# Optimization experiments

Hardware: AMD Instinct MI355X
Metric: run time of the kernel (lower is better)

Reference implementation:

```python
import jax, jax.numpy as jnp
import numpy as np

EMBED_DIM = 768
NUM_HEADS = 12
HEAD_DIM = EMBED_DIM // NUM_HEADS
SCALER = HEAD_DIM ** (-0.5)


def setup_inputs() -> dict:
    key = jax.random.key(0)
    k_x, k_wqkv, k_wo = jax.random.split(key, 3)
    B, N, C = 8, 1024, EMBED_DIM
    # GlorotUniform limits
    lim_qkv = (6.0 / (C + 3 * C)) ** 0.5
    lim_o = (6.0 / (C + C)) ** 0.5
    return {
        "inputs": jax.random.normal(k_x, (B, N, C), dtype=jnp.float32),
        "w_qkv": jax.random.uniform(k_wqkv, (C, 3 * C), minval=-lim_qkv, maxval=lim_qkv, dtype=jnp.float32),
        "b_qkv": jnp.zeros((3 * C,), dtype=jnp.float32),
        "w_out": jax.random.uniform(k_wo, (C, C), minval=-lim_o, maxval=lim_o, dtype=jnp.float32),
        "b_out": jnp.zeros((C,), dtype=jnp.float32),
    }


def reference(inputs, w_qkv, b_qkv, w_out, b_out):
    B, N, C = inputs.shape
    H, D = NUM_HEADS, C // NUM_HEADS
    qkv = inputs @ w_qkv + b_qkv                      # [B, N, 3C]
    qkv = qkv.reshape(B, N, 3, H, D).transpose(2, 0, 3, 1, 4)  # [3, B, H, N, D]
    q, k, v = qkv[0], qkv[1], qkv[2]
    scores = jnp.einsum("bhnd,bhmd->bhnm", q, k) * SCALER      # [B, H, N, N]
    attn = jax.nn.softmax(scores, axis=-1)
    x = jnp.einsum("bhnm,bhmd->bhnd", attn, v)                  # [B, H, N, D]
    x = x.transpose(0, 2, 1, 3).reshape(B, N, C)
    return x @ w_out + b_out
```

## Files before the change

### kernel.cpp

```cpp
#include <hip/hip_runtime.h>
#include <hip/hip_bf16.h>
#include <cstdint>
#include <cstddef>

#define EMBED 768
#define NHEADS 12
#define HDIM 64
#define SEQ 1024
#define BATCH 8

typedef __attribute__((ext_vector_type(8))) short bf16x8;
typedef __attribute__((ext_vector_type(4))) float f32x4;
typedef __attribute__((ext_vector_type(16))) float f32x16;
typedef __attribute__((ext_vector_type(4))) unsigned int u32x4;

__device__ __forceinline__ short f2bf(float f) {
    union { float f; uint32_t u; } x; x.f = f;
    uint32_t r = x.u + 0x7fffu + ((x.u >> 16) & 1u);
    return (short)(r >> 16);
}

__device__ __forceinline__ unsigned int cvt_pk_bf16(float lo, float hi) {
    unsigned int r;
    asm("v_cvt_pk_bf16_f32 %0, %1, %2" : "=v"(r) : "v"(lo), "v"(hi));
    return r;
}

__device__ __forceinline__ void permswap(unsigned int& a, unsigned int& b) {
    asm volatile("v_permlane32_swap_b32 %0, %1" : "+v"(a), "+v"(b));
}

__device__ __forceinline__ void gload_lds16(const void* g, void* l) {
    __builtin_amdgcn_global_load_lds(
        (const __attribute__((address_space(1))) unsigned int*)g,
        (__attribute__((address_space(3))) unsigned int*)l, 16, 0, 0);
}

__global__ __launch_bounds__(256) void prep(
    const float* __restrict__ x, short* __restrict__ Xbf,
    const float* __restrict__ w_qkv, short* __restrict__ wqkvT,
    const float* __restrict__ w_out, short* __restrict__ woutT) {
    __shared__ float tile[64][65];
    const int tid = threadIdx.x;
    const int bidx = blockIdx.x;
    if (bidx < 3072) {
        size_t i = ((size_t)bidx * 256 + tid) * 8;
        float4 a = *reinterpret_cast<const float4*>(x + i);
        float4 b = *reinterpret_cast<const float4*>(x + i + 4);
        bf16x8 v;
        v[0] = f2bf(a.x); v[1] = f2bf(a.y); v[2] = f2bf(a.z); v[3] = f2bf(a.w);
        v[4] = f2bf(b.x); v[5] = f2bf(b.y); v[6] = f2bf(b.z); v[7] = f2bf(b.w);
        *reinterpret_cast<bf16x8*>(Xbf + i) = v;
        return;
    }
    const float* in;
    short* out;
    int R, C, c0, r0;
    if (bidx < 3504) {
        int bid = bidx - 3072;
        in = w_qkv; out = wqkvT; R = 768; C = 2304;
        c0 = (bid % 36) * 64; r0 = (bid / 36) * 64;
    } else {
        int bid = bidx - 3504;
        in = w_out; out = woutT; R = 768; C = 768;
        c0 = (bid % 12) * 64; r0 = (bid / 12) * 64;
    }
#pragma unroll
    for (int i = 0; i < 16; ++i) {
        int e = tid + 256 * i;
        int r = e >> 6, c = e & 63;
        tile[r][c] = in[(size_t)(r0 + r) * C + c0 + c];
    }
    __syncthreads();
#pragma unroll
    for (int i = 0; i < 16; ++i) {
        int e = tid + 256 * i;
        int rr = e >> 6, cc = e & 63;
        out[(size_t)(c0 + rr) * R + r0 + cc] = f2bf(tile[cc][rr]);
    }
}

__global__ __launch_bounds__(512) void gemm_qkv(
    const short* __restrict__ A, const short* __restrict__ Bt,
    const float* __restrict__ bias,
    short* __restrict__ Qo, short* __restrict__ Ko, short* __restrict__ Vto) {
    __shared__ __align__(16) char smem[65536];
    const int tid = threadIdx.x;
    const int lane = tid & 63;
    const int wid = tid >> 6;
    const int wm = wid >> 1, wn = wid & 1;
    const int bid = blockIdx.x;
    const int wg = (bid & 7) * 144 + (bid >> 3);
    const int mb = wg / 18, nb = wg - mb * 18;
    const int m0 = mb * 128;
    const int n0 = nb * 128;

    const f32x4 zero4 = {0.f, 0.f, 0.f, 0.f};
    f32x4 acc[2][4];
#pragma unroll
    for (int i = 0; i < 2; ++i)
#pragma unroll
        for (int j = 0; j < 4; ++j) acc[i][j] = zero4;

    const short* Ab = A + (size_t)m0 * EMBED;
    const short* Bb = Bt + (size_t)n0 * EMBED;

    auto stage = [&](int p, int kt) {
        const int k0 = kt * 64;
        char* base = smem + p * 32768;
#pragma unroll
        for (int i = 0; i < 2; ++i) {
            int e = i * 512 + tid;
            int r = e >> 3, cs = (e & 7) ^ (r & 7);
            char* dst = base + (size_t)(i * 512 + wid * 64) * 16;
            gload_lds16(Ab + (size_t)r * EMBED + k0 + cs * 8, dst);
            gload_lds16(Bb + (size_t)r * EMBED + k0 + cs * 8, dst + 16384);
        }
    };

    stage(0, 0);
    stage(1, 1);
    asm volatile("s_waitcnt vmcnt(4)" ::: "memory");
    __builtin_amdgcn_s_barrier();
    __builtin_amdgcn_sched_barrier(0);

    for (int t = 0; t < 12; ++t) {
        const int p = t & 1;
        const char* As = smem + p * 32768;
        const char* Bs = As + 16384;
        bf16x8 af[2][2], bfv[4][2];
#pragma unroll
        for (int mi = 0; mi < 2; ++mi)
#pragma unroll
            for (int kh = 0; kh < 2; ++kh) {
                int row = wm * 32 + mi * 16 + (lane & 15);
                int c = kh * 4 + (lane >> 4);
                af[mi][kh] = *reinterpret_cast<const bf16x8*>(
                    As + row * 128 + (((c ^ (row & 7))) << 4));
            }
#pragma unroll
        for (int ni = 0; ni < 4; ++ni)
#pragma unroll
            for (int kh = 0; kh < 2; ++kh) {
                int row = wn * 64 + ni * 16 + (lane & 15);
                int c = kh * 4 + (lane >> 4);
                bfv[ni][kh] = *reinterpret_cast<const bf16x8*>(
                    Bs + row * 128 + (((c ^ (row & 7))) << 4));
            }
        asm volatile("s_waitcnt lgkmcnt(0)" ::: "memory");
        __builtin_amdgcn_s_barrier();
        __builtin_amdgcn_sched_barrier(0);
        if (t + 2 < 12) stage(p, t + 2);

        __builtin_amdgcn_s_setprio(1);
#pragma unroll
        for (int mi = 0; mi < 2; ++mi)
#pragma unroll
            for (int ni = 0; ni < 4; ++ni)
#pragma unroll
                for (int kh = 0; kh < 2; ++kh)
                    acc[mi][ni] = __builtin_amdgcn_mfma_f32_16x16x32_bf16(
                        af[mi][kh], bfv[ni][kh], acc[mi][ni], 0, 0, 0);
        __builtin_amdgcn_s_setprio(0);

        if (t + 2 < 12)
            asm volatile("s_waitcnt vmcnt(4)" ::: "memory");
        else
            asm volatile("s_waitcnt vmcnt(0)" ::: "memory");
        __builtin_amdgcn_s_barrier();
        __builtin_amdgcn_sched_barrier(0);
    }

    const int s = nb / 6;
    const int bb = m0 >> 10;
    if (s == 2) {
        char* T = smem;
#pragma unroll
        for (int mi = 0; mi < 2; ++mi)
#pragma unroll
            for (int ni = 0; ni < 4; ++ni)
#pragma unroll
                for (int rp = 0; rp < 2; ++rp) {
                    int ml = wm * 32 + mi * 16 + ((lane >> 4) << 2) + rp * 2;
                    int nl = wn * 64 + ni * 16 + (lane & 15);
                    float bsv = bias[n0 + nl];
                    unsigned int w = cvt_pk_bf16(acc[mi][ni][rp * 2] + bsv,
                                                 acc[mi][ni][rp * 2 + 1] + bsv);
                    *reinterpret_cast<unsigned int*>(
                        T + nl * 256 + ((ml * 2) ^ ((nl & 7) << 4))) = w;
                }
        __syncthreads();
        short* Vrow0 = Vto + ((size_t)bb * 768 + (nb - 12) * 128) * SEQ + (m0 & 1023);
#pragma unroll
        for (int it = 0; it < 4; ++it) {
            int chunk = it * 512 + tid;
            int row = chunk >> 4, k = chunk & 15;
            u32x4 v = *reinterpret_cast<const u32x4*>(
                T + row * 256 + ((k * 16) ^ ((row & 7) << 4)));
            *reinterpret_cast<u32x4*>(Vrow0 + (size_t)row * SEQ + k * 8) = v;
        }
    } else {
        short* dst = (s == 0) ? Qo : Ko;
        const float qs = (s == 0) ? 0.18033688f : 1.0f;
        const int rem0 = n0 - s * 768;
#pragma unroll
        for (int mi = 0; mi < 2; ++mi)
#pragma unroll
            for (int ni = 0; ni < 4; ++ni)
#pragma unroll
                for (int r = 0; r < 4; ++r) {
                    int m = m0 + wm * 32 + mi * 16 + ((lane >> 4) << 2) + r;
                    int nl = wn * 64 + ni * 16 + (lane & 15);
                    int rem = rem0 + nl;
                    int h = rem >> 6, d = rem & 63;
                    int tok = m & 1023;
                    float v = (acc[mi][ni][r] + bias[n0 + nl]) * qs;
                    dst[(((size_t)(bb * NHEADS + h)) * SEQ + tok) * HDIM + d] = f2bf(v);
                }
    }
}

__global__ __launch_bounds__(128, 2) void attn_kernel(
    const short* __restrict__ Q, const short* __restrict__ K,
    const short* __restrict__ Vt, short* __restrict__ Xo) {
    __shared__ __align__(16) char smem[49152];
    const int tid = threadIdx.x, lane = tid & 63, wid = tid >> 6;
    const int l31 = lane & 31, g = lane >> 5;
    const int bh = blockIdx.x, qt = blockIdx.y;
    const int b = bh / NHEADS, h = bh - b * NHEADS;
    const short* Qh = Q + (size_t)bh * SEQ * HDIM;
    const short* Kh = K + (size_t)bh * SEQ * HDIM;
    const short* Vh = Vt + (size_t)bh * HDIM * SEQ;
    const int q0 = qt * 128 + wid * 64;
    const int swz = (l31 & 7);

    const f32x16 zero16 = 0.f;
    bf16x8 qf[2][4];
#pragma unroll
    for (int qg = 0; qg < 2; ++qg)
#pragma unroll
        for (int ds = 0; ds < 4; ++ds)
            qf[qg][ds] = *reinterpret_cast<const bf16x8*>(
                Qh + (size_t)(q0 + qg * 32 + l31) * HDIM + ds * 16 + g * 8);

    f32x16 oA0 = zero16, oA1 = zero16, oB0 = zero16, oB1 = zero16;
    float lA = 0.f, lB = 0.f;

    auto stage = [&](int buf, int j0) {
#pragma unroll
        for (int i = 0; i < 4; ++i) {
            int e = i * 128 + tid;
            int r = e >> 3, cs = (e & 7) ^ (r & 7);
            char* dst = smem + (size_t)(i * 128 + wid * 64) * 16 + buf * 8192;
            gload_lds16(Kh + (size_t)(j0 + r) * HDIM + cs * 8, dst);
            gload_lds16(Vh + (size_t)r * SEQ + j0 + cs * 8, dst + 24576);
        }
    };

    stage(0, 0);
    stage(1, 64);

    for (int t = 0; t < 16; ++t) {
        const int bsel = t % 3;
        if (t < 15)
            asm volatile("s_waitcnt vmcnt(8)" ::: "memory");
        else
            asm volatile("s_waitcnt vmcnt(0)" ::: "memory");
        __builtin_amdgcn_s_barrier();
        __builtin_amdgcn_sched_barrier(0);

        const char* kb = smem + bsel * 8192;
        const char* vb = smem + 24576 + bsel * 8192;

        bf16x8 kf[2][4];
#pragma unroll
        for (int s = 0; s < 2; ++s)
#pragma unroll
            for (int ds = 0; ds < 4; ++ds)
                kf[s][ds] = *reinterpret_cast<const bf16x8*>(
                    kb + (s * 32 + l31) * 128 + (((ds * 2 + g) ^ swz) << 4));

        f32x16 sA0 = zero16, sA1 = zero16, sB0 = zero16, sB1 = zero16;
        __builtin_amdgcn_s_setprio(1);
#pragma unroll
        for (int ds = 0; ds < 4; ++ds) {
            sA0 = __builtin_amdgcn_mfma_f32_32x32x16_bf16(kf[0][ds], qf[0][ds], sA0, 0, 0, 0);
            sA1 = __builtin_amdgcn_mfma_f32_32x32x16_bf16(kf[1][ds], qf[0][ds], sA1, 0, 0, 0);
            sB0 = __builtin_amdgcn_mfma_f32_32x32x16_bf16(kf[0][ds], qf[1][ds], sB0, 0, 0, 0);
            sB1 = __builtin_amdgcn_mfma_f32_32x32x16_bf16(kf[1][ds], qf[1][ds], sB1, 0, 0, 0);
        }
        __builtin_amdgcn_s_setprio(0);

        float rsA = 0.f, rsB = 0.f;
#pragma unroll
        for (int r = 0; r < 16; ++r) {
            float a0 = __builtin_amdgcn_exp2f(sA0[r]);
            float a1 = __builtin_amdgcn_exp2f(sA1[r]);
            float b0 = __builtin_amdgcn_exp2f(sB0[r]);
            float b1 = __builtin_amdgcn_exp2f(sB1[r]);
            sA0[r] = a0; sA1[r] = a1; sB0[r] = b0; sB1[r] = b1;
            rsA += a0 + a1; rsB += b0 + b1;
        }
        lA += rsA; lB += rsB;

        bf16x8 pfA[4], pfB[4];
#pragma unroll
        for (int qg = 0; qg < 2; ++qg) {
            bf16x8* pf = qg ? pfB : pfA;
#pragma unroll
            for (int s = 0; s < 2; ++s) {
                const f32x16& sv = qg ? (s ? sB1 : sB0) : (s ? sA1 : sA0);
                unsigned int pk[8];
#pragma unroll
                for (int j = 0; j < 8; ++j) pk[j] = cvt_pk_bf16(sv[2 * j], sv[2 * j + 1]);
                permswap(pk[0], pk[2]); permswap(pk[1], pk[3]);
                permswap(pk[4], pk[6]); permswap(pk[5], pk[7]);
                u32x4 wlo, whi;
                wlo[0] = pk[0]; wlo[1] = pk[1]; wlo[2] = pk[2]; wlo[3] = pk[3];
                whi[0] = pk[4]; whi[1] = pk[5]; whi[2] = pk[6]; whi[3] = pk[7];
                pf[s * 2 + 0] = __builtin_bit_cast(bf16x8, wlo);
                pf[s * 2 + 1] = __builtin_bit_cast(bf16x8, whi);
            }
        }

        bf16x8 vf[4][2];
#pragma unroll
        for (int kst = 0; kst < 4; ++kst)
#pragma unroll
            for (int dsub = 0; dsub < 2; ++dsub)
                vf[kst][dsub] = *reinterpret_cast<const bf16x8*>(
                    vb + (dsub * 32 + l31) * 128 + (((kst * 2 + g) ^ swz) << 4));
        __builtin_amdgcn_sched_barrier(0);
        if (t + 2 < 16) stage((t + 2) % 3, (t + 2) * 64);

        __builtin_amdgcn_s_setprio(1);
#pragma unroll
        for (int kst = 0; kst < 4; ++kst) {
            oA0 = __builtin_amdgcn_mfma_f32_32x32x16_bf16(vf[kst][0], pfA[kst], oA0, 0, 0, 0);
            oA1 = __builtin_amdgcn_mfma_f32_32x32x16_bf16(vf[kst][1], pfA[kst], oA1, 0, 0, 0);
            oB0 = __builtin_amdgcn_mfma_f32_32x32x16_bf16(vf[kst][0], pfB[kst], oB0, 0, 0, 0);
            oB1 = __builtin_amdgcn_mfma_f32_32x32x16_bf16(vf[kst][1], pfB[kst], oB1, 0, 0, 0);
        }
        __builtin_amdgcn_s_setprio(0);
    }

    lA += __shfl_xor(lA, 32);
    lB += __shfl_xor(lB, 32);
    const float rlA = 1.0f / lA, rlB = 1.0f / lB;

    __syncthreads();
    char* T = smem;
    {
        const int qx = (l31 & 7) << 4;
#pragma unroll
        for (int qg = 0; qg < 2; ++qg) {
            char* Tw = T + (wid * 64 + qg * 32 + l31) * 128;
            const float rl = qg ? rlB : rlA;
#pragma unroll
            for (int half = 0; half < 2; ++half) {
                const f32x16& ov = qg ? (half ? oB1 : oB0) : (half ? oA1 : oA0);
#pragma unroll
                for (int j = 0; j < 8; ++j) {
                    unsigned int w = cvt_pk_bf16(ov[2 * j] * rl, ov[2 * j + 1] * rl);
                    int off = 4 * (j & 1) + 16 * (j >> 1) + 8 * g + 64 * half;
                    *reinterpret_cast<unsigned int*>(Tw + (off ^ qx)) = w;
                }
            }
        }
    }
    __syncthreads();
    const int q0b = qt * 128;
    short* xbase = Xo + ((size_t)b * SEQ + q0b) * EMBED + h * HDIM;
#pragma unroll
    for (int it = 0; it < 8; ++it) {
        int chunk = it * 128 + tid;
        int row = chunk >> 3, k = chunk & 7;
        u32x4 v = *reinterpret_cast<const u32x4*>(
            T + row * 128 + ((k * 16) ^ ((row & 7) << 4)));
        *reinterpret_cast<u32x4*>(xbase + (size_t)row * EMBED + k * 8) = v;
    }
}

__global__ __launch_bounds__(256) void gemm_out(
    const short* __restrict__ A, const short* __restrict__ Bt,
    const float* __restrict__ bias, float* __restrict__ C) {
    __shared__ __align__(16) char smem[49152];
    const int tid = threadIdx.x;
    const int lane = tid & 63;
    const int wid = tid >> 6;
    const int wm = wid >> 1, wn = wid & 1;
    const int bid = blockIdx.x;
    const int wg = (bid & 7) * 96 + (bid >> 3);
    const int mb = wg / 12, nb = wg - mb * 12;
    const int m0 = mb * 128;
    const int n0 = nb * 64;

    const f32x4 zero4 = {0.f, 0.f, 0.f, 0.f};
    f32x4 acc[4][2];
#pragma unroll
    for (int i = 0; i < 4; ++i)
#pragma unroll
        for (int j = 0; j < 2; ++j) acc[i][j] = zero4;

    const short* Ab = A + (size_t)m0 * EMBED;
    const short* Bb = Bt + (size_t)n0 * EMBED;

    auto stage = [&](int p, int kt) {
        const int k0 = kt * 64;
        char* base = smem + p * 24576;
#pragma unroll
        for (int i = 0; i < 4; ++i) {
            int e = i * 256 + tid;
            int r = e >> 3, cs = (e & 7) ^ (r & 7);
            gload_lds16(Ab + (size_t)r * EMBED + k0 + cs * 8,
                        base + (size_t)(i * 256 + wid * 64) * 16);
        }
#pragma unroll
        for (int i = 0; i < 2; ++i) {
            int e = i * 256 + tid;
            int r = e >> 3, cs = (e & 7) ^ (r & 7);
            gload_lds16(Bb + (size_t)r * EMBED + k0 + cs * 8,
                        base + 16384 + (size_t)(i * 256 + wid * 64) * 16);
        }
    };

    stage(0, 0);
    stage(1, 1);
    asm volatile("s_waitcnt vmcnt(6)" ::: "memory");
    __builtin_amdgcn_s_barrier();
    __builtin_amdgcn_sched_barrier(0);

    for (int t = 0; t < 12; ++t) {
        const int p = t & 1;
        const char* As = smem + p * 24576;
        const char* Bs = As + 16384;
        bf16x8 af[4][2], bfv[2][2];
#pragma unroll
        for (int mi = 0; mi < 4; ++mi)
#pragma unroll
            for (int kh = 0; kh < 2; ++kh) {
                int row = wm * 64 + mi * 16 + (lane & 15);
                int c = kh * 4 + (lane >> 4);
                af[mi][kh] = *reinterpret_cast<const bf16x8*>(
                    As + row * 128 + (((c ^ (row & 7))) << 4));
            }
#pragma unroll
        for (int ni = 0; ni < 2; ++ni)
#pragma unroll
            for (int kh = 0; kh < 2; ++kh) {
                int row = wn * 32 + ni * 16 + (lane & 15);
                int c = kh * 4 + (lane >> 4);
                bfv[ni][kh] = *reinterpret_cast<const bf16x8*>(
                    Bs + row * 128 + (((c ^ (row & 7))) << 4));
            }
        asm volatile("s_waitcnt lgkmcnt(0)" ::: "memory");
        __builtin_amdgcn_s_barrier();
        __builtin_amdgcn_sched_barrier(0);
        if (t + 2 < 12) stage(p, t + 2);

        __builtin_amdgcn_s_setprio(1);
#pragma unroll
        for (int mi = 0; mi < 4; ++mi)
#pragma unroll
            for (int ni = 0; ni < 2; ++ni)
#pragma unroll
                for (int kh = 0; kh < 2; ++kh)
                    acc[mi][ni] = __builtin_amdgcn_mfma_f32_16x16x32_bf16(
                        af[mi][kh], bfv[ni][kh], acc[mi][ni], 0, 0, 0);
        __builtin_amdgcn_s_setprio(0);

        if (t + 2 < 12)
            asm volatile("s_waitcnt vmcnt(6)" ::: "memory");
        else
            asm volatile("s_waitcnt vmcnt(0)" ::: "memory");
        __builtin_amdgcn_s_barrier();
        __builtin_amdgcn_sched_barrier(0);
    }

#pragma unroll
    for (int mi = 0; mi < 4; ++mi)
#pragma unroll
        for (int ni = 0; ni < 2; ++ni)
#pragma unroll
            for (int r = 0; r < 4; ++r) {
                int m = m0 + wm * 64 + mi * 16 + ((lane >> 4) << 2) + r;
                int n = n0 + wn * 32 + ni * 16 + (lane & 15);
                C[(size_t)m * EMBED + n] = acc[mi][ni][r] + bias[n];
            }
}

extern "C" void kernel_launch(void* const* d_in, const int* in_sizes, int n_in,
                              void* d_out, int out_size, void* d_ws, size_t ws_size,
                              hipStream_t stream) {
    const float* x      = (const float*)d_in[0];
    const float* w_qkv  = (const float*)d_in[1];
    const float* b_qkv  = (const float*)d_in[2];
    const float* w_out  = (const float*)d_in[3];
    const float* b_out  = (const float*)d_in[4];
    float* out = (float*)d_out;
    char* ws = (char*)d_ws;

    short* wqkvT = (short*)(ws + 0);
    short* woutT = (short*)(ws + 3538944);
    short* Qb    = (short*)(ws + 4718592);
    short* Kb    = (short*)(ws + 17301504);
    short* Vtb   = (short*)(ws + 29884416);
    short* Xbf   = (short*)(ws + 42467328);
    short* Xab   = (short*)(ws + 42467328);

    prep<<<dim3(3648), 256, 0, stream>>>(x, Xbf, w_qkv, wqkvT, w_out, woutT);
    gemm_qkv<<<dim3(1152), 512, 0, stream>>>(Xbf, wqkvT, b_qkv, Qb, Kb, Vtb);
    attn_kernel<<<dim3(96, 8), 128, 0, stream>>>(Qb, Kb, Vtb, Xab);
    gemm_out<<<dim3(768), 256, 0, stream>>>(Xab, woutT, b_out, out);
}
```

Before: 101.6 us.

## Split attention inner loop into per-query-group phases to overlap exp with MFMA

Reorders the attention inner loop so the V-fragment loads and the next K/V staging are issued before the QK^T MFMAs. The A and B query groups are then processed in separate phases: the exp2/convert work for group A can overlap with MFMAs for group B, and PV for A runs before B's softmax. The goal is to interleave VALU exp work with matrix-core work and hide LDS and global latency. It may raise register pressure or let the compiler reorder things differently than intended.

```diff
diff --git a/kernel.cpp b/kernel.cpp
--- a/kernel.cpp
+++ b/kernel.cpp
@@ -279,50 +279,6 @@
             for (int ds = 0; ds < 4; ++ds)
                 kf[s][ds] = *reinterpret_cast<const bf16x8*>(
                     kb + (s * 32 + l31) * 128 + (((ds * 2 + g) ^ swz) << 4));
-
-        f32x16 sA0 = zero16, sA1 = zero16, sB0 = zero16, sB1 = zero16;
-        __builtin_amdgcn_s_setprio(1);
-#pragma unroll
-        for (int ds = 0; ds < 4; ++ds) {
-            sA0 = __builtin_amdgcn_mfma_f32_32x32x16_bf16(kf[0][ds], qf[0][ds], sA0, 0, 0, 0);
-            sA1 = __builtin_amdgcn_mfma_f32_32x32x16_bf16(kf[1][ds], qf[0][ds], sA1, 0, 0, 0);
-            sB0 = __builtin_amdgcn_mfma_f32_32x32x16_bf16(kf[0][ds], qf[1][ds], sB0, 0, 0, 0);
-            sB1 = __builtin_amdgcn_mfma_f32_32x32x16_bf16(kf[1][ds], qf[1][ds], sB1, 0, 0, 0);
-        }
-        __builtin_amdgcn_s_setprio(0);
-
-        float rsA = 0.f, rsB = 0.f;
-#pragma unroll
-        for (int r = 0; r < 16; ++r) {
-            float a0 = __builtin_amdgcn_exp2f(sA0[r]);
-            float a1 = __builtin_amdgcn_exp2f(sA1[r]);
-            float b0 = __builtin_amdgcn_exp2f(sB0[r]);
-            float b1 = __builtin_amdgcn_exp2f(sB1[r]);
-            sA0[r] = a0; sA1[r] = a1; sB0[r] = b0; sB1[r] = b1;
-            rsA += a0 + a1; rsB += b0 + b1;
-        }
-        lA += rsA; lB += rsB;
-
-        bf16x8 pfA[4], pfB[4];
-#pragma unroll
-        for (int qg = 0; qg < 2; ++qg) {
-            bf16x8* pf = qg ? pfB : pfA;
-#pragma unroll
-            for (int s = 0; s < 2; ++s) {
-                const f32x16& sv = qg ? (s ? sB1 : sB0) : (s ? sA1 : sA0);
-                unsigned int pk[8];
-#pragma unroll
-                for (int j = 0; j < 8; ++j) pk[j] = cvt_pk_bf16(sv[2 * j], sv[2 * j + 1]);
-                permswap(pk[0], pk[2]); permswap(pk[1], pk[3]);
-                permswap(pk[4], pk[6]); permswap(pk[5], pk[7]);
-                u32x4 wlo, whi;
-                wlo[0] = pk[0]; wlo[1] = pk[1]; wlo[2] = pk[2]; wlo[3] = pk[3];
-                whi[0] = pk[4]; whi[1] = pk[5]; whi[2] = pk[6]; whi[3] = pk[7];
-                pf[s * 2 + 0] = __builtin_bit_cast(bf16x8, wlo);
-                pf[s * 2 + 1] = __builtin_bit_cast(bf16x8, whi);
-            }
-        }
-
         bf16x8 vf[4][2];
 #pragma unroll
         for (int kst = 0; kst < 4; ++kst)
@@ -333,11 +289,80 @@
         __builtin_amdgcn_sched_barrier(0);
         if (t + 2 < 16) stage((t + 2) % 3, (t + 2) * 64);
 
+        f32x16 sA0 = zero16, sA1 = zero16;
+        __builtin_amdgcn_s_setprio(1);
+#pragma unroll
+        for (int ds = 0; ds < 4; ++ds) {
+            sA0 = __builtin_amdgcn_mfma_f32_32x32x16_bf16(kf[0][ds], qf[0][ds], sA0, 0, 0, 0);
+            sA1 = __builtin_amdgcn_mfma_f32_32x32x16_bf16(kf[1][ds], qf[0][ds], sA1, 0, 0, 0);
+        }
+        __builtin_amdgcn_s_setprio(0);
+        f32x16 sB0 = zero16, sB1 = zero16;
+        __builtin_amdgcn_s_setprio(1);
+#pragma unroll
+        for (int ds = 0; ds < 4; ++ds) {
+            sB0 = __builtin_amdgcn_mfma_f32_32x32x16_bf16(kf[0][ds], qf[1][ds], sB0, 0, 0, 0);
+            sB1 = __builtin_amdgcn_mfma_f32_32x32x16_bf16(kf[1][ds], qf[1][ds], sB1, 0, 0, 0);
+        }
+        __builtin_amdgcn_s_setprio(0);
+
+        float rsA = 0.f;
+#pragma unroll
+        for (int r = 0; r < 16; ++r) {
+            float a0 = __builtin_amdgcn_exp2f(sA0[r]);
+            float a1 = __builtin_amdgcn_exp2f(sA1[r]);
+            sA0[r] = a0; sA1[r] = a1; rsA += a0 + a1;
+        }
+        lA += rsA;
+        bf16x8 pfA[4];
+#pragma unroll
+        for (int s = 0; s < 2; ++s) {
+            const f32x16& sv = s ? sA1 : sA0;
+            unsigned int pk[8];
+#pragma unroll
+            for (int j = 0; j < 8; ++j) pk[j] = cvt_pk_bf16(sv[2 * j], sv[2 * j + 1]);
+            permswap(pk[0], pk[2]); permswap(pk[1], pk[3]);
+            permswap(pk[4], pk[6]); permswap(pk[5], pk[7]);
+            u32x4 wlo, whi;
+            wlo[0] = pk[0]; wlo[1] = pk[1]; wlo[2] = pk[2]; wlo[3] = pk[3];
+            whi[0] = pk[4]; whi[1] = pk[5]; whi[2] = pk[6]; whi[3] = pk[7];
+            pfA[s * 2 + 0] = __builtin_bit_cast(bf16x8, wlo);
+            pfA[s * 2 + 1] = __builtin_bit_cast(bf16x8, whi);
+        }
         __builtin_amdgcn_s_setprio(1);
 #pragma unroll
         for (int kst = 0; kst < 4; ++kst) {
             oA0 = __builtin_amdgcn_mfma_f32_32x32x16_bf16(vf[kst][0], pfA[kst], oA0, 0, 0, 0);
             oA1 = __builtin_amdgcn_mfma_f32_32x32x16_bf16(vf[kst][1], pfA[kst], oA1, 0, 0, 0);
+        }
+        __builtin_amdgcn_s_setprio(0);
+
+        float rsB = 0.f;
+#pragma unroll
+        for (int r = 0; r < 16; ++r) {
+            float b0 = __builtin_amdgcn_exp2f(sB0[r]);
+            float b1 = __builtin_amdgcn_exp2f(sB1[r]);
+            sB0[r] = b0; sB1[r] = b1; rsB += b0 + b1;
+        }
+        lB += rsB;
+        bf16x8 pfB[4];
+#pragma unroll
+        for (int s = 0; s < 2; ++s) {
+            const f32x16& sv = s ? sB1 : sB0;
+            unsigned int pk[8];
+#pragma unroll
+            for (int j = 0; j < 8; ++j) pk[j] = cvt_pk_bf16(sv[2 * j], sv[2 * j + 1]);
+            permswap(pk[0], pk[2]); permswap(pk[1], pk[3]);
+            permswap(pk[4], pk[6]); permswap(pk[5], pk[7]);
+            u32x4 wlo, whi;
+            wlo[0] = pk[0]; wlo[1] = pk[1]; wlo[2] = pk[2]; wlo[3] = pk[3];
+            whi[0] = pk[4]; whi[1] = pk[5]; whi[2] = pk[6]; whi[3] = pk[7];
+            pfB[s * 2 + 0] = __builtin_bit_cast(bf16x8, wlo);
+            pfB[s * 2 + 1] = __builtin_bit_cast(bf16x8, whi);
+        }
+        __builtin_amdgcn_s_setprio(1);
+#pragma unroll
+        for (int kst = 0; kst < 4; ++kst) {
             oB0 = __builtin_amdgcn_mfma_f32_32x32x16_bf16(vf[kst][0], pfB[kst], oB0, 0, 0, 0);
             oB1 = __builtin_amdgcn_mfma_f32_32x32x16_bf16(vf[kst][1], pfB[kst], oB1, 0, 0, 0);
         }
```

Measured after the change: 99.76 us. About the same (-1.8%).
